# Optimization experiments

Hardware: AMD Instinct MI355X
Metric: run time of the kernel (lower is better)

The kernel has to match this reference:

```python
import jax, jax.numpy as jnp
import numpy as np
from jax import lax

B, N, M, C = 32, 4096, 256, 91
EPS = 1e-7  # torchvision giou_loss eps
NEG_INF = -jnp.inf


def _make_boxes(key, b, n):
    # valid xyxy boxes in [0,1]
    kc, ks = jax.random.split(key)
    c = jax.random.uniform(kc, (b, n, 2), minval=0.1, maxval=0.9)
    wh = jax.random.uniform(ks, (b, n, 2), minval=0.02, maxval=0.2)
    return jnp.concatenate([c - wh / 2, c + wh / 2], axis=-1)


def setup_inputs() -> dict:
    key = jax.random.key(0)
    k1, k2, k3, k4 = jax.random.split(key, 4)
    return {
        "pr_boxes": _make_boxes(k1, B, N),
        "gt_boxes": _make_boxes(k2, B, M),
        "pr_class_logits": jax.random.normal(k3, (B, N, C), dtype=jnp.float32),
        "gt_classes": jax.random.randint(k4, (B, M), 0, C),
    }


def _box_iou(a, b):
    # a: [N,4], b: [M,4] xyxy -> [N,M] (torchvision.ops.box_iou)
    lt = jnp.maximum(a[:, None, :2], b[None, :, :2])
    rb = jnp.minimum(a[:, None, 2:], b[None, :, 2:])
    wh = jnp.clip(rb - lt, 0.0)
    inter = wh[..., 0] * wh[..., 1]
    area_a = (a[:, 2] - a[:, 0]) * (a[:, 3] - a[:, 1])
    area_b = (b[:, 2] - b[:, 0]) * (b[:, 3] - b[:, 1])
    union = area_a[:, None] + area_b[None, :] - inter
    return inter / union


def _match(pr, gt):
    # greedy maximal-IoU matching: sequentially take global argmax, mask row+col
    ious = _box_iou(pr, gt)  # [N, M]

    def step(ious, _):
        idx = jnp.argmax(ious)
        i, j = idx // M, idx % M
        ious = ious.at[i, :].set(NEG_INF).at[:, j].set(NEG_INF)
        return ious, (i, j)

    _, (pr_idx, gt_order) = lax.scan(step, ious, None, length=M)
    pr_mask = jnp.zeros((N,), dtype=bool).at[pr_idx].set(True)
    return pr_idx, gt_order, pr_mask


def _giou_loss_mean(b1, b2):
    # elementwise generalized_box_iou_loss, reduction='mean' (torchvision)
    xi1 = jnp.maximum(b1[:, 0], b2[:, 0])
    yi1 = jnp.maximum(b1[:, 1], b2[:, 1])
    xi2 = jnp.minimum(b1[:, 2], b2[:, 2])
    yi2 = jnp.minimum(b1[:, 3], b2[:, 3])
    inter = jnp.clip(xi2 - xi1, 0.0) * jnp.clip(yi2 - yi1, 0.0)
    area1 = (b1[:, 2] - b1[:, 0]) * (b1[:, 3] - b1[:, 1])
    area2 = (b2[:, 2] - b2[:, 0]) * (b2[:, 3] - b2[:, 1])
    union = area1 + area2 - inter
    iou = inter / (union + EPS)
    xc1 = jnp.minimum(b1[:, 0], b2[:, 0])
    yc1 = jnp.minimum(b1[:, 1], b2[:, 1])
    xc2 = jnp.maximum(b1[:, 2], b2[:, 2])
    yc2 = jnp.maximum(b1[:, 3], b2[:, 3])
    area_c = (xc2 - xc1) * (yc2 - yc1)
    giou = iou - (area_c - union) / (area_c + EPS)
    return jnp.mean(1.0 - giou)


def reference(pr_boxes, gt_boxes, pr_class_logits, gt_classes):
    pr_idx, gt_order, pr_mask = jax.vmap(_match)(pr_boxes, gt_boxes)  # [B,M],[B,M],[B,N]
    # unmatched prediction indices (fixed count N-M)
    neg_idx = jax.vmap(lambda m: jnp.nonzero(~m, size=N - M)[0])(pr_mask)  # [B, N-M]

    pr_pos = jnp.take_along_axis(pr_boxes, pr_idx[..., None], axis=1)   # [B,M,4]
    gt_pos = jnp.take_along_axis(gt_boxes, gt_order[..., None], axis=1)  # [B,M,4]
    pr_neg = jnp.take_along_axis(pr_boxes, neg_idx[..., None], axis=1)  # [B,N-M,4]
    gt_neg = jnp.zeros_like(pr_neg)

    l_loss = (jax.vmap(_giou_loss_mean)(pr_pos, gt_pos).sum()
              + jax.vmap(_giou_loss_mean)(pr_neg, gt_neg).sum())
    # c_loss is never accumulated in the original module (classification branch is dead code)
    c_loss = 0.0
    count = pr_boxes.shape[0]
    return (c_loss + l_loss) / count / 2.0
```

## Files before the change

kernel.cpp:

```cpp
#include <hip/hip_runtime.h>

#pragma clang fp contract(off)

#define NBOX 4096
#define MBOX 256
#define NBATCH 32
#define GEPS 1e-7f
#define DEPTH 12
#define RDEPTH 8

typedef unsigned long long u64;
typedef unsigned int u32;
typedef unsigned short u16;

#define OFF_PRS   0
#define OFF_TOP   65536
#define OFF_G     90112
#define OFF_GAR   94208
#define OFF_MATCH 95232
#define LDS_BYTES 96256

__device__ __forceinline__ u64 shfl_u64(u64 x, int src) {
  u32 lo = (u32)x, hi = (u32)(x >> 32);
  lo = __shfl(lo, src, 64);
  hi = __shfl(hi, src, 64);
  return ((u64)hi << 32) | (u64)lo;
}

__device__ __forceinline__ u32 wave_max_u32(u32 x) {
#define DPPL32(CTRL)                                                            \
  {                                                                             \
    u32 s = (u32)__builtin_amdgcn_update_dpp(0, (int)x, CTRL, 0xf, 0xf, true);  \
    x = x > s ? x : s;                                                          \
  }
  DPPL32(0xB1) DPPL32(0x4E) DPPL32(0x141) DPPL32(0x140) DPPL32(0x142) DPPL32(0x143)
#undef DPPL32
  return (u32)__builtin_amdgcn_readlane((int)x, 63);
}

__device__ __forceinline__ u64 wave_max_colkey(u64 key) {
  u32 iou = (u32)(key >> 13);
  u32 maxiou = wave_max_u32(iou);
  u32 tb = (iou == maxiou) ? ((u32)key & 0x1FFFu) : 0u;
  u32 maxtb = wave_max_u32(tb);
  return ((u64)maxiou << 13) | (u64)maxtb;
}

__device__ __forceinline__ u32 iou_bits(float4 a, float areaA, float4 g, float gar) {
  #pragma clang fp contract(off)
  float w = fminf(a.z, g.z) - fmaxf(a.x, g.x);
  float h = fminf(a.w, g.w) - fmaxf(a.y, g.y);
  w = fmaxf(w, 0.0f);
  h = fmaxf(h, 0.0f);
  float inter = w * h;
  float uni = (areaA + gar) - inter;
  float v = inter / uni;
  return __float_as_uint(v);
}

__device__ __forceinline__ float giou_loss(float ax1, float ay1, float ax2, float ay2,
                                           float bx1, float by1, float bx2, float by2) {
  #pragma clang fp contract(off)
  float xi1 = fmaxf(ax1, bx1), yi1 = fmaxf(ay1, by1);
  float xi2 = fminf(ax2, bx2), yi2 = fminf(ay2, by2);
  float inter = fmaxf(xi2 - xi1, 0.0f) * fmaxf(yi2 - yi1, 0.0f);
  float area1 = (ax2 - ax1) * (ay2 - ay1);
  float area2 = (bx2 - bx1) * (by2 - by1);
  float uni = (area1 + area2) - inter;
  float iou = inter / (uni + GEPS);
  float xc1 = fminf(ax1, bx1), yc1 = fminf(ay1, by1);
  float xc2 = fmaxf(ax2, bx2), yc2 = fmaxf(ay2, by2);
  float areac = (xc2 - xc1) * (yc2 - yc1);
  float giou = iou - (areac - uni) / (areac + GEPS);
  return 1.0f - giou;
}


__global__ __launch_bounds__(256) __attribute__((amdgpu_waves_per_eu(1, 6)))
void init_cols(const float4* __restrict__ pr, const float4* __restrict__ gt,
               u64* __restrict__ topG) {
  const int blk = blockIdx.x;
  const int b = blk >> 6, cg = blk & 63;
  const int tid = threadIdx.x, lane = tid & 63, wid = tid >> 6;
  const int j = cg * 4 + wid;
  const float4* prb = pr + (size_t)b * NBOX;
  float4 gb = gt[(size_t)b * MBOX + j];
  float gar = (gb.z - gb.x) * (gb.w - gb.y);

  u64 t0 = 0ull, t1 = 0ull, t2 = 0ull, dm = 0ull;
  for (int k = 0; k < 64; ++k) {
    int r = (k << 6) + lane;
    float4 a = prb[r];
    float areaA = (a.z - a.x) * (a.w - a.y);
    u64 key = ((u64)iou_bits(a, areaA, gb, gar) << 13) | (u64)(NBOX - r);
    bool c0 = key > t0, c1 = key > t1, c2 = key > t2;
    u64 d = c2 ? t2 : key;
    if (d > dm) dm = d;
    u64 n1 = c1 ? (c0 ? t0 : key) : t1;
    u64 n2 = c2 ? (c1 ? t1 : key) : t2;
    t0 = c0 ? key : t0;
    t1 = n1;
    t2 = n2;
  }
  u64* out = topG + ((size_t)b * MBOX + j) * DEPTH;
  int h = 0;
  u64 m12 = 0ull;
  for (int e = 0; e < DEPTH; ++e) {
    u64 cand = (h == 0) ? t0 : (h == 1) ? t1 : (h == 2) ? t2 : 0ull;
    u64 m = wave_max_colkey(cand);
    if (cand == m && m) h++;
    if (lane == 0) out[e] = m;
    m12 = m;
  }
  if (__ballot(dm > m12) != 0ull) {
    u64 t[DEPTH];
    #pragma unroll
    for (int q = 0; q < DEPTH; ++q) t[q] = 0ull;
    for (int k = 0; k < 64; ++k) {
      int r = (k << 6) + lane;
      float4 a = prb[r];
      float areaA = (a.z - a.x) * (a.w - a.y);
      u64 key = ((u64)iou_bits(a, areaA, gb, gar) << 13) | (u64)(NBOX - r);
      if (key > t[DEPTH - 1]) {
        t[DEPTH - 1] = key;
        #pragma unroll
        for (int q = DEPTH - 1; q > 0; --q)
          if (t[q] > t[q - 1]) { u64 tmp = t[q]; t[q] = t[q - 1]; t[q - 1] = tmp; }
      }
    }
    int h2 = 0;
    for (int e = 0; e < DEPTH; ++e) {
      u64 cand = 0;
      #pragma unroll
      for (int q = 0; q < DEPTH; ++q) if (q == h2) cand = t[q];
      u64 m = wave_max_colkey(cand);
      if (cand == m && m) h2++;
      if (lane == 0) out[e] = m;
    }
  }
}

__global__ __launch_bounds__(64) __attribute__((amdgpu_waves_per_eu(1, 4)))
void greedy_kernel(const float4* __restrict__ pr, const float4* __restrict__ gt,
                   const u64* __restrict__ topG, float* __restrict__ partial) {
  extern __shared__ char smem[];
  float4* prs  = (float4*)(smem + OFF_PRS);
  u64* top     = (u64*)(smem + OFF_TOP);
  float4* g    = (float4*)(smem + OFF_G);
  float* garea = (float*)(smem + OFF_GAR);
  u32* match   = (u32*)(smem + OFF_MATCH);

  const int b = blockIdx.x;
  const int lane = threadIdx.x;
  const float4* prb = pr + (size_t)b * NBOX;

  float negdiff = 0.0f, possum = 0.0f, negsub = 0.0f;
  for (int k = 0; k < 64; ++k) {
    int r = (k << 6) + lane;
    float4 a = prb[r];
    prs[r] = a;
    negdiff += giou_loss(a.x, a.y, a.z, a.w, 0.0f, 0.0f, 0.0f, 0.0f);
  }
  #pragma unroll
  for (int k = 0; k < 4; ++k) {
    int j = (k << 6) + lane;
    float4 gg = gt[(size_t)b * MBOX + j];
    g[j] = gg;
    garea[j] = (gg.z - gg.x) * (gg.w - gg.y);
  }
  {
    float4* dst = (float4*)top;
    const float4* src = (const float4*)(topG + (size_t)b * MBOX * DEPTH);
    for (int k = 0; k < MBOX * DEPTH / 2 / 64; ++k) dst[(k << 6) + lane] = src[(k << 6) + lane];
  }
  u64 rowlive = ~0ull;
  u64 cb[4];
  u64 la[4];
  u64 cfc[4];
  u32 posreg = 0x02020202u;
  #pragma unroll
  for (int q = 0; q < 4; ++q) {
    int j = (q << 6) + lane;
    cfc[q] = (u64)(MBOX - j);
    u64 e0 = top[j * DEPTH];
    u64 e1 = top[j * DEPTH + 1];
    cb[q] = ((e0 >> 13) << 22) | ((e0 & 0x1FFFull) << 9) | cfc[q];
    la[q] = e1;
  }

  for (int step = 0; step < MBOX; ++step) {
    u64 m0 = cb[0] > cb[1] ? cb[0] : cb[1];
    u64 m1 = cb[2] > cb[3] ? cb[2] : cb[3];
    u64 mb = m0 > m1 ? m0 : m1;
    u32 iou32 = (u32)(mb >> 22);
    u32 maxiou = wave_max_u32(iou32);
    u32 tb = (iou32 == maxiou) ? ((u32)mb & 0x3FFFFFu) : 0u;
    u32 maxtb = wave_max_u32(tb);
    if (lane == 0) match[step] = maxtb;
    if (step == MBOX - 1) break;
    const u32 rfield = (maxtb >> 9) & 0x1FFFu;
    const int i = NBOX - (int)rfield;
    u64 kill = (lane == (i & 63)) ? (1ull << (i >> 6)) : 0ull;
    rowlive &= ~kill;
    u32 walkmask = 0;
    #pragma unroll
    for (int q = 0; q < 4; ++q) {
      u32 lo22 = (u32)cb[q] & 0x3FFFFFu;
      bool aff = (lo22 >> 9) == rfield;
      bool ismatch = (lo22 == maxtb);
      if (aff && ismatch) cb[q] = 0ull;
      if (aff && !ismatch) walkmask |= (1u << q);
    }
    u64 wb = __ballot(walkmask != 0);
    if (wb != 0ull) {
      u32 need = walkmask;
      u32 exmask = 0;
      for (;;) {
        #pragma unroll
        for (int q = 0; q < 4; ++q) {
          u64 e = la[q];
          int r = NBOX - (int)(e & 0x1FFFull);
          u64 rl = shfl_u64(rowlive, r & 63);
          if ((need >> q) & 1) {
            if (e == 0ull) {
              cb[q] = 0ull;
              need &= ~(1u << q);
              exmask |= (1u << q);
            } else if ((rl >> ((r >> 6) & 63)) & 1ull) {
              cb[q] = ((e >> 13) << 22) | ((e & 0x1FFFull) << 9) | cfc[q];
              need &= ~(1u << q);
              int p = (int)((posreg >> (q * 8)) & 0xFFu);
              la[q] = (p < DEPTH) ? top[((q << 6) + lane) * DEPTH + p] : 0ull;
              posreg = (posreg & ~(0xFFu << (q * 8))) | ((u32)(p + 1) << (q * 8));
            } else {
              int p = (int)((posreg >> (q * 8)) & 0xFFu);
              la[q] = (p < DEPTH) ? top[((q << 6) + lane) * DEPTH + p] : 0ull;
              posreg = (posreg & ~(0xFFu << (q * 8))) | ((u32)(p + 1) << (q * 8));
            }
          }
        }
        if (__ballot(need != 0) == 0ull) break;
      }
      u64 exb = __ballot(exmask != 0);
      while (exb != 0ull) {
        const int src = (int)__ffsll((unsigned long long)exb) - 1;
        const u32 em = (u32)__shfl((int)exmask, src, 64);
        const int q = __ffs(em) - 1;
        const int jj = (q << 6) + src;
        if (lane == src) exmask &= ~(1u << q);
        exb = __ballot(exmask != 0);
        float4 gb = g[jj];
        float gar = garea[jj];
        u64 t[RDEPTH];
        #pragma unroll
        for (int z = 0; z < RDEPTH; ++z) t[z] = 0ull;
        for (int k = 0; k < 64; ++k) {
          if ((rowlive >> k) & 1ull) {
            int rr = (k << 6) + lane;
            float4 a = prs[rr];
            float areaA = (a.z - a.x) * (a.w - a.y);
            u64 key = ((u64)iou_bits(a, areaA, gb, gar) << 13) | (u64)(NBOX - rr);
            if (key > t[RDEPTH - 1]) {
              t[RDEPTH - 1] = key;
              #pragma unroll
              for (int z = RDEPTH - 1; z > 0; --z)
                if (t[z] > t[z - 1]) { u64 tmp = t[z]; t[z] = t[z - 1]; t[z - 1] = tmp; }
            }
          }
        }
        u64 ent0 = 0ull, ent1 = 0ull;
        int h = 0;
        for (int e = 0; e < RDEPTH; ++e) {
          u64 cand = 0;
          #pragma unroll
          for (int z = 0; z < RDEPTH; ++z) if (z == h) cand = t[z];
          u64 mm = wave_max_colkey(cand);
          if (cand == mm && mm) h++;
          if (e == 0) ent0 = mm;
          if (e == 1) ent1 = mm;
          if (lane == 0) top[jj * DEPTH + e] = mm;
        }
        if (lane >= RDEPTH && lane < DEPTH) top[jj * DEPTH + lane] = 0ull;
        if (lane == src) {
          cb[q] = ((ent0 >> 13) << 22) | ((ent0 & 0x1FFFull) << 9) | cfc[q];
          la[q] = ent1;
          posreg = (posreg & ~(0xFFu << (q * 8))) | (2u << (q * 8));
        }
      }
    }
  }

  #pragma unroll
  for (int t4 = 0; t4 < 4; ++t4) {
    int s = (t4 << 6) + lane;
    u32 mm = match[s];
    int i = NBOX - (int)(mm >> 9);
    int j = MBOX - (int)(mm & 0x1FFu);
    float4 a = prs[i];
    float4 gg = g[j];
    possum += giou_loss(a.x, a.y, a.z, a.w, gg.x, gg.y, gg.z, gg.w);
    negsub += giou_loss(a.x, a.y, a.z, a.w, 0.0f, 0.0f, 0.0f, 0.0f);
  }

  #pragma unroll
  for (int o = 32; o; o >>= 1) {
    possum  += __shfl_xor(possum, o, 64);
    negsub  += __shfl_xor(negsub, o, 64);
    negdiff += __shfl_xor(negdiff, o, 64);
  }
  if (lane == 0)
    partial[b] = possum / 256.0f + (negdiff - negsub) / 3840.0f;
}

__global__ void finalize_kernel(const float* __restrict__ partial, float* __restrict__ out) {
  if (threadIdx.x == 0) {
    float s = 0.0f;
    for (int i = 0; i < NBATCH; ++i) s += partial[i];
    out[0] = s / 64.0f;
  }
}

extern "C" void kernel_launch(void* const* d_in, const int* in_sizes, int n_in,
                              void* d_out, int out_size, void* d_ws, size_t ws_size,
                              hipStream_t stream) {
  (void)in_sizes; (void)n_in; (void)out_size; (void)ws_size;
  const float4* pr = (const float4*)d_in[0];
  const float4* gt = (const float4*)d_in[1];
  char* ws = (char*)d_ws;
  u64* topG = (u64*)ws;
  float* partial = (float*)(ws + (size_t)NBATCH * MBOX * DEPTH * 8);
  float* out = (float*)d_out;

  hipFuncSetAttribute((const void*)greedy_kernel,
                      hipFuncAttributeMaxDynamicSharedMemorySize, LDS_BYTES);

  hipLaunchKernelGGL(init_cols, dim3(NBATCH * 64), dim3(256), 0, stream, pr, gt, topG);
  hipLaunchKernelGGL(greedy_kernel, dim3(NBATCH), dim3(64), LDS_BYTES, stream,
                     pr, gt, topG, partial);
  hipLaunchKernelGGL(finalize_kernel, dim3(1), dim3(64), 0, stream, partial, out);
}
```

Before: 167.2 us.

## Commit two greedy matches per iteration when second-best column uses a different row

The greedy matching loop now computes the runner-up candidate after excluding the winning column and, if its row differs from the winner's row, commits it as the next match in the same iteration. This roughly halves the number of serial wave-wide reductions and repair walks when pairs are independent. It costs an extra pair of wave reductions and some per-lane second-max bookkeeping per iteration, and correctness depends on the second candidate still being the global maximum after the first row is removed.

```diff
diff --git a/kernel.cpp b/kernel.cpp
--- a/kernel.cpp
+++ b/kernel.cpp
@@ -44,6 +44,13 @@
   u32 tb = (iou == maxiou) ? ((u32)key & 0x1FFFu) : 0u;
   u32 maxtb = wave_max_u32(tb);
   return ((u64)maxiou << 13) | (u64)maxtb;
+}
+
+__device__ __forceinline__ u32 wave_max_globalkey(u64 key) {
+  u32 iou = (u32)(key >> 22);
+  u32 maxiou = wave_max_u32(iou);
+  u32 tb = (iou == maxiou) ? ((u32)key & 0x3FFFFFu) : 0u;
+  return wave_max_u32(tb);
 }
 
 __device__ __forceinline__ u32 iou_bits(float4 a, float areaA, float4 g, float gar) {
@@ -188,26 +195,43 @@
     la[q] = e1;
   }
 
-  for (int step = 0; step < MBOX; ++step) {
-    u64 m0 = cb[0] > cb[1] ? cb[0] : cb[1];
-    u64 m1 = cb[2] > cb[3] ? cb[2] : cb[3];
-    u64 mb = m0 > m1 ? m0 : m1;
-    u32 iou32 = (u32)(mb >> 22);
-    u32 maxiou = wave_max_u32(iou32);
-    u32 tb = (iou32 == maxiou) ? ((u32)mb & 0x3FFFFFu) : 0u;
-    u32 maxtb = wave_max_u32(tb);
-    if (lane == 0) match[step] = maxtb;
-    if (step == MBOX - 1) break;
-    const u32 rfield = (maxtb >> 9) & 0x1FFFu;
-    const int i = NBOX - (int)rfield;
-    u64 kill = (lane == (i & 63)) ? (1ull << (i >> 6)) : 0ull;
-    rowlive &= ~kill;
+  int step = 0;
+  while (step < MBOX) {
+    u64 hi01 = cb[0] > cb[1] ? cb[0] : cb[1];
+    u64 lo01 = cb[0] > cb[1] ? cb[1] : cb[0];
+    u64 hi23 = cb[2] > cb[3] ? cb[2] : cb[3];
+    u64 lo23 = cb[2] > cb[3] ? cb[3] : cb[2];
+    u64 mb1 = hi01 > hi23 ? hi01 : hi23;
+    u64 sec = hi01 > hi23 ? (lo01 > hi23 ? lo01 : hi23)
+                          : (lo23 > hi01 ? lo23 : hi01);
+    u32 maxtb1 = wave_max_globalkey(mb1);
+    if (lane == 0) match[step] = maxtb1;
+    step++;
+    if (step == MBOX) break;
+    const u32 rf1 = (maxtb1 >> 9) & 0x1FFFu;
+    const int i1 = NBOX - (int)rf1;
+    u64 cand2 = (((u32)mb1 & 0x3FFFFFu) == maxtb1 && mb1 != 0ull) ? sec : mb1;
+    u32 maxtb2 = wave_max_globalkey(cand2);
+    const u32 rf2 = (maxtb2 >> 9) & 0x1FFFu;
+    const bool dbl = (maxtb2 != 0u) && (rf2 != rf1);
+    u32 rfB = rf1;
+    if (dbl) {
+      if (lane == 0) match[step] = maxtb2;
+      step++;
+      rfB = rf2;
+    }
+    if (step == MBOX) break;
+    const int i2 = NBOX - (int)rfB;
+    u64 kill1 = (lane == (i1 & 63)) ? (1ull << (i1 >> 6)) : 0ull;
+    u64 kill2 = (lane == (i2 & 63)) ? (1ull << (i2 >> 6)) : 0ull;
+    rowlive &= ~(kill1 | kill2);
     u32 walkmask = 0;
     #pragma unroll
     for (int q = 0; q < 4; ++q) {
       u32 lo22 = (u32)cb[q] & 0x3FFFFFu;
-      bool aff = (lo22 >> 9) == rfield;
-      bool ismatch = (lo22 == maxtb);
+      u32 rfq = lo22 >> 9;
+      bool aff = (rfq == rf1) | (rfq == rfB);
+      bool ismatch = (lo22 == maxtb1) | (dbl & (lo22 == maxtb2));
       if (aff && ismatch) cb[q] = 0ull;
       if (aff && !ismatch) walkmask |= (1u << q);
     }
```

After: 172.8 us. 3.3% more time.
